# Kernel tuning notes

Measured on AMD Instinct MI355X. Metric: run time of the kernel, lower is better.

The kernel has to match this reference:

```python
import jax, jax.numpy as jnp
import numpy as np

N = 100000
F_IN = 128
H = 128
E = 1600000
EP = 200000


def _gcn_conv(x, W, b, src, dst, n):
    # GCNConv (PyG default): add self-loops done by caller; symmetric norm; linear + scatter-add.
    xw = x @ W                                        # [n, H]
    deg = jax.ops.segment_sum(jnp.ones(src.shape[0], x.dtype), dst, num_segments=n)
    dinv = jnp.where(deg > 0, jax.lax.rsqrt(deg), 0.0)
    norm = dinv[src] * dinv[dst]                      # [E']
    msg = xw[src] * norm[:, None]                     # [E', H] gather
    out = jax.ops.segment_sum(msg, dst, num_segments=n)  # scatter-add
    return out + b


def setup_inputs() -> dict:
    key = jax.random.key(0)
    k = jax.random.split(key, 9)
    x = jax.random.normal(k[0], (N, F_IN), dtype=jnp.float32)
    edge_index = jax.random.randint(k[1], (2, E), 0, N, dtype=jnp.int64)
    dict_node = jax.random.randint(k[2], (N,), 0, N, dtype=jnp.int64)
    pos_edge_index = jax.random.randint(k[3], (2, EP), 0, N, dtype=jnp.int64)
    neg_edge_index = jax.random.randint(k[4], (2, EP), 0, N, dtype=jnp.int64)
    s1 = 1.0 / np.sqrt(F_IN)
    s2 = 1.0 / np.sqrt(H)
    W1 = jax.random.uniform(k[5], (F_IN, H), jnp.float32, -s1, s1)
    b1 = jnp.zeros((H,), jnp.float32)
    W2 = jax.random.uniform(k[6], (H, H), jnp.float32, -s2, s2)
    b2 = jnp.zeros((H,), jnp.float32)
    return {"x": x, "W1": W1, "b1": b1, "W2": W2, "b2": b2,
            "edge_index": edge_index, "dict_node": dict_node,
            "pos_edge_index": pos_edge_index, "neg_edge_index": neg_edge_index}


def reference(x, W1, b1, W2, b2, edge_index, dict_node, pos_edge_index, neg_edge_index):
    n = x.shape[0]
    # add self-loops once (both convs use the same edge_index)
    loop = jnp.arange(n, dtype=edge_index.dtype)
    src = jnp.concatenate([edge_index[0], loop])
    dst = jnp.concatenate([edge_index[1], loop])
    # encode (dropout p=0.01 is identity in eval mode)
    h = jax.nn.relu(_gcn_conv(x, W1, b1, src, dst, n))
    h = jax.nn.relu(_gcn_conv(h, W2, b2, src, dst, n))
    # global_mean_pool over dict_node segments (size = num_nodes)
    sums = jax.ops.segment_sum(h, dict_node, num_segments=n)
    cnt = jax.ops.segment_sum(jnp.ones((n,), h.dtype), dict_node, num_segments=n)
    z = sums / jnp.maximum(cnt, 1.0)[:, None]
    # decode: per-edge dot products over concatenated pos/neg edges
    ei = jnp.concatenate([pos_edge_index, neg_edge_index], axis=-1)
    logits = jnp.sum(z[ei[0]] * z[ei[1]], axis=-1)
    return logits
```

## Files before the change

kernel.cpp:

```cpp
#include <hip/hip_runtime.h>
#include <hip/hip_fp16.h>

#define HH 128
#define PCHUNK 16384


__global__ __launch_bounds__(256) void part_count_k(const int* __restrict__ key, int e,
                                                    int nbkt, int nblk,
                                                    int* __restrict__ gcnt,
                                                    int* __restrict__ blkoff) {
  __shared__ int h[512];
  for (int i = threadIdx.x; i < nbkt; i += 256) h[i] = 0;
  __syncthreads();
  int start = blockIdx.x * PCHUNK;
  int cnt = e - start; if (cnt > PCHUNK) cnt = PCHUNK;
  for (int i = threadIdx.x; i < cnt; i += 256)
    atomicAdd(&h[key[start + i] >> 8], 1);
  __syncthreads();
  for (int i = threadIdx.x; i < nbkt; i += 256) {
    int c = h[i];
    if (c) blkoff[(size_t)i * nblk + blockIdx.x] = atomicAdd(&gcnt[i], c);
  }
}

__global__ __launch_bounds__(512) void scan_bkt_k(const int* __restrict__ gcnt,
                                                  int* __restrict__ bktbase, int nbkt, int e) {
  __shared__ int sc[512];
  int tid = threadIdx.x;
  int v = (tid < nbkt) ? gcnt[tid] : 0;
  sc[tid] = v;
  __syncthreads();
  for (int off = 1; off < 512; off <<= 1) {
    int t = (tid >= off) ? sc[tid - off] : 0;
    __syncthreads();
    sc[tid] += t;
    __syncthreads();
  }
  if (tid < nbkt) bktbase[tid] = sc[tid] - v;
  if (tid == 0) bktbase[nbkt] = e;
}

__global__ __launch_bounds__(256) void part_scatter_k(const int* __restrict__ src,
                                                      const int* __restrict__ key, int e,
                                                      int nbkt, int nblk,
                                                      const int* __restrict__ bktbase,
                                                      const int* __restrict__ blkoff,
                                                      int* __restrict__ part) {
  __shared__ int cur[512];
  for (int i = threadIdx.x; i < nbkt; i += 256)
    cur[i] = bktbase[i] + blkoff[(size_t)i * nblk + blockIdx.x];
  __syncthreads();
  int start = blockIdx.x * PCHUNK;
  int cnt = e - start; if (cnt > PCHUNK) cnt = PCHUNK;
  for (int i = threadIdx.x; i < cnt; i += 256) {
    int d = key[start + i], s = src[start + i];
    int pos = atomicAdd(&cur[d >> 8], 1);
    part[pos] = (s << 8) | (d & 255);
  }
}

__global__ __launch_bounds__(256) void part_scatter_idx_k(const int* __restrict__ key, int e,
                                                          int nbkt, int nblk,
                                                          const int* __restrict__ bktbase,
                                                          const int* __restrict__ blkoff,
                                                          int* __restrict__ part) {
  __shared__ int cur[512];
  for (int i = threadIdx.x; i < nbkt; i += 256)
    cur[i] = bktbase[i] + blkoff[(size_t)i * nblk + blockIdx.x];
  __syncthreads();
  int start = blockIdx.x * PCHUNK;
  int cnt = e - start; if (cnt > PCHUNK) cnt = PCHUNK;
  for (int i = threadIdx.x; i < cnt; i += 256) {
    int d = key[start + i];
    int pos = atomicAdd(&cur[d >> 8], 1);
    part[pos] = ((start + i) << 8) | (d & 255);
  }
}

__global__ __launch_bounds__(256) void bucket_csr_k(const int* __restrict__ part,
                                                    const int* __restrict__ bktbase,
                                                    int* __restrict__ rowptr,
                                                    float* __restrict__ dinv,
                                                    int* __restrict__ esrc,
                                                    int n, int e, int nbkt) {
  __shared__ int hist[256];
  __shared__ int sc[256];
  __shared__ int cur[256];
  int tid = threadIdx.x;
  int b = blockIdx.x;
  int dstbase = b << 8;
  int nloc = n - dstbase; if (nloc > 256) nloc = 256;
  int beg = bktbase[b], bend = bktbase[b + 1];

  hist[tid] = 0;
  __syncthreads();
  for (int j = beg + tid; j < bend; j += 256)
    atomicAdd(&hist[part[j] & 255], 1);
  __syncthreads();
  int v = hist[tid];
  sc[tid] = v;
  __syncthreads();
  for (int off = 1; off < 256; off <<= 1) {
    int t = (tid >= off) ? sc[tid - off] : 0;
    __syncthreads();
    sc[tid] += t;
    __syncthreads();
  }
  int excl = sc[tid] - v;
  if (tid < nloc) {
    rowptr[dstbase + tid] = beg + excl;
    cur[tid] = beg + excl;
    if (dinv) dinv[dstbase + tid] = rsqrtf((float)v + 1.0f);
  }
  __syncthreads();
  for (int j = beg + tid; j < bend; j += 256) {
    int p = part[j];
    int pos = atomicAdd(&cur[p & 255], 1);
    esrc[pos] = p >> 8;
  }
  if (b == nbkt - 1 && tid == 0) rowptr[n] = e;
}

template <bool OUT16>
__global__ __launch_bounds__(256) void gemm128_v4(const float* __restrict__ A,
                                                  const float* __restrict__ W,
                                                  const float* __restrict__ dscale,
                                                  void* __restrict__ out, int n) {
  __shared__ float As[64][65];
  const int tid = threadIdx.x;
  const int rbase = blockIdx.x * 64;
  const int vrows = (n - rbase) < 64 ? (n - rbase) : 64;

  const int r = tid & 63;
  const int q = __builtin_amdgcn_readfirstlane(tid >> 6);
  const float* Wq = W + q * 32;

  float4 acc[8];
  #pragma unroll
  for (int c = 0; c < 8; ++c) acc[c] = make_float4(0.f, 0.f, 0.f, 0.f);

  #pragma unroll
  for (int ph = 0; ph < 2; ++ph) {
    if (ph) __syncthreads();
    #pragma unroll
    for (int j = 0; j < 4; ++j) {
      int f = tid + 256 * j;
      int rr = f >> 4, c4 = f & 15;
      float4 v = (rr < vrows)
          ? ((const float4*)(A + (size_t)(rbase + rr) * HH + ph * 64))[c4]
          : make_float4(0.f, 0.f, 0.f, 0.f);
      As[rr][c4 * 4 + 0] = v.x;
      As[rr][c4 * 4 + 1] = v.y;
      As[rr][c4 * 4 + 2] = v.z;
      As[rr][c4 * 4 + 3] = v.w;
    }
    __syncthreads();

    #pragma unroll 4
    for (int kk = 0; kk < 64; ++kk) {
      float a = As[r][kk];
      const float4* Wr = (const float4*)(Wq + (size_t)(ph * 64 + kk) * HH);
      #pragma unroll
      for (int c = 0; c < 8; ++c) {
        float4 w = Wr[c];
        acc[c].x += a * w.x; acc[c].y += a * w.y;
        acc[c].z += a * w.z; acc[c].w += a * w.w;
      }
    }
  }

  int row = rbase + r;
  if (row < n) {
    float s = dscale ? dscale[row] : 1.0f;
    if (OUT16) {
      uint2* o = (uint2*)((__half*)out + (size_t)row * HH) + q * 8;
      #pragma unroll
      for (int c = 0; c < 8; ++c) {
        __half2 h0 = __float22half2_rn(make_float2(acc[c].x * s, acc[c].y * s));
        __half2 h1 = __float22half2_rn(make_float2(acc[c].z * s, acc[c].w * s));
        uint2 u;
        u.x = *reinterpret_cast<unsigned*>(&h0);
        u.y = *reinterpret_cast<unsigned*>(&h1);
        o[c] = u;
      }
    } else {
      float4* o = (float4*)((float*)out + (size_t)row * HH + q * 32);
      #pragma unroll
      for (int c = 0; c < 8; ++c) {
        acc[c].x *= s; acc[c].y *= s; acc[c].z *= s; acc[c].w *= s;
        o[c] = acc[c];
      }
    }
  }
}

template <bool HOUT16>
__global__ __launch_bounds__(256) void gather16_k(const __half* __restrict__ xw16,
                                                  const int* __restrict__ rowptr,
                                                  const int* __restrict__ esrc,
                                                  const float* __restrict__ dinv,
                                                  const float* __restrict__ bias,
                                                  void* __restrict__ h, int n) {
  int wid = (int)((blockIdx.x * (size_t)blockDim.x + threadIdx.x) >> 6);
  int lane = threadIdx.x & 63;
  if (wid >= n) return;
  int beg = rowptr[wid], end = rowptr[wid + 1];
  int half = lane >> 5, l32 = lane & 31;
  const uint2* base = (const uint2*)xw16 + l32;
  float4 acc = make_float4(0.f, 0.f, 0.f, 0.f);

  for (int j0 = beg; j0 < end; j0 += 64) {
    int myj = j0 + lane;
    int sv = (myj < end) ? esrc[myj] : 0;
    int cnt = end - j0; if (cnt > 64) cnt = 64;
    int k = 0;
    for (; k + 8 <= cnt; k += 8) {
      #pragma unroll
      for (int p = 0; p < 4; ++p) {
        int sa = __builtin_amdgcn_readlane(sv, k + 2 * p);
        int sb = __builtin_amdgcn_readlane(sv, k + 2 * p + 1);
        unsigned off = (unsigned)(half ? sb : sa) << 5;
        uint2 u = base[off];
        float2 f0 = __half22float2(*reinterpret_cast<__half2*>(&u.x));
        float2 f1 = __half22float2(*reinterpret_cast<__half2*>(&u.y));
        acc.x += f0.x; acc.y += f0.y; acc.z += f1.x; acc.w += f1.y;
      }
    }
    for (; k + 2 <= cnt; k += 2) {
      int sa = __builtin_amdgcn_readlane(sv, k);
      int sb = __builtin_amdgcn_readlane(sv, k + 1);
      unsigned off = (unsigned)(half ? sb : sa) << 5;
      uint2 u = base[off];
      float2 f0 = __half22float2(*reinterpret_cast<__half2*>(&u.x));
      float2 f1 = __half22float2(*reinterpret_cast<__half2*>(&u.y));
      acc.x += f0.x; acc.y += f0.y; acc.z += f1.x; acc.w += f1.y;
    }
    if (k < cnt) {
      int sa = __builtin_amdgcn_readlane(sv, k);
      if (half == 0) {
        uint2 u = base[(unsigned)sa << 5];
        float2 f0 = __half22float2(*reinterpret_cast<__half2*>(&u.x));
        float2 f1 = __half22float2(*reinterpret_cast<__half2*>(&u.y));
        acc.x += f0.x; acc.y += f0.y; acc.z += f1.x; acc.w += f1.y;
      }
    }
  }
  acc.x += __shfl_xor(acc.x, 32);
  acc.y += __shfl_xor(acc.y, 32);
  acc.z += __shfl_xor(acc.z, 32);
  acc.w += __shfl_xor(acc.w, 32);
  if (half == 0) {
    uint2 u = base[(unsigned)wid << 5];
    float2 s0 = __half22float2(*reinterpret_cast<__half2*>(&u.x));
    float2 s1 = __half22float2(*reinterpret_cast<__half2*>(&u.y));
    float di = dinv[wid];
    float4 bb = ((const float4*)bias)[l32];
    float4 o;
    o.x = fmaxf(bb.x + di * (acc.x + s0.x), 0.f);
    o.y = fmaxf(bb.y + di * (acc.y + s0.y), 0.f);
    o.z = fmaxf(bb.z + di * (acc.z + s1.x), 0.f);
    o.w = fmaxf(bb.w + di * (acc.w + s1.y), 0.f);
    if (HOUT16) {
      __half2 p0 = __float22half2_rn(make_float2(o.x, o.y));
      __half2 p1 = __float22half2_rn(make_float2(o.z, o.w));
      uint2 w;
      w.x = *reinterpret_cast<unsigned*>(&p0);
      w.y = *reinterpret_cast<unsigned*>(&p1);
      ((uint2*)h)[((size_t)wid << 5) + l32] = w;
    } else {
      ((float4*)h)[((size_t)wid << 5) + l32] = o;
    }
  }
}

__global__ __launch_bounds__(256) void pool16_k(const __half* __restrict__ h2,
                                                const int* __restrict__ rowptr,
                                                const int* __restrict__ nodelist,
                                                __half* __restrict__ z, int n) {
  int gid = blockIdx.x * blockDim.x + threadIdx.x;
  int g = gid >> 5, l32 = gid & 31;
  if (g >= n) return;
  int beg = rowptr[g], end = rowptr[g + 1];
  const uint2* h4 = (const uint2*)h2;
  float4 a = make_float4(0.f, 0.f, 0.f, 0.f);
  for (int j = beg; j < end; ++j) {
    int m = nodelist[j];
    uint2 u = h4[((size_t)m << 5) + l32];
    float2 f0 = __half22float2(*reinterpret_cast<__half2*>(&u.x));
    float2 f1 = __half22float2(*reinterpret_cast<__half2*>(&u.y));
    a.x += f0.x; a.y += f0.y; a.z += f1.x; a.w += f1.y;
  }
  float inv = 1.0f / fmaxf((float)(end - beg), 1.0f);
  __half2 p0 = __float22half2_rn(make_float2(a.x * inv, a.y * inv));
  __half2 p1 = __float22half2_rn(make_float2(a.z * inv, a.w * inv));
  uint2 w;
  w.x = *reinterpret_cast<unsigned*>(&p0);
  w.y = *reinterpret_cast<unsigned*>(&p1);
  ((uint2*)z)[((size_t)g << 5) + l32] = w;
}

__global__ __launch_bounds__(256) void decode16_k(const __half* __restrict__ z,
                                                  const int* __restrict__ pos,
                                                  const int* __restrict__ neg,
                                                  float* __restrict__ out, int ep) {
  int gid = blockIdx.x * blockDim.x + threadIdx.x;
  int edge = gid >> 5, l32 = gid & 31;
  if (edge >= 2 * ep) return;
  int a, b;
  if (edge < ep) { a = pos[edge];      b = pos[ep + edge]; }
  else           { int t = edge - ep; a = neg[t]; b = neg[ep + t]; }
  const uint2* z4 = (const uint2*)z;
  uint2 ua = z4[((size_t)a << 5) + l32];
  uint2 ub = z4[((size_t)b << 5) + l32];
  float2 fa0 = __half22float2(*reinterpret_cast<__half2*>(&ua.x));
  float2 fa1 = __half22float2(*reinterpret_cast<__half2*>(&ua.y));
  float2 fb0 = __half22float2(*reinterpret_cast<__half2*>(&ub.x));
  float2 fb1 = __half22float2(*reinterpret_cast<__half2*>(&ub.y));
  float dot = fa0.x * fb0.x + fa0.y * fb0.y + fa1.x * fb1.x + fa1.y * fb1.y;
  #pragma unroll
  for (int off = 16; off > 0; off >>= 1) dot += __shfl_xor(dot, off);
  if (l32 == 0) out[edge] = dot;
}

__global__ void fill_deg_k(float* __restrict__ deg, int n) {
  int i = blockIdx.x * blockDim.x + threadIdx.x;
  if (i < n) deg[i] = 1.0f;
}
__global__ void accum_deg_k(const int* __restrict__ dst, float* __restrict__ deg, int e) {
  int i = blockIdx.x * blockDim.x + threadIdx.x;
  if (i < e) atomicAdd(&deg[dst[i]], 1.0f);
}
__global__ void dinv_k(float* __restrict__ deg, int n) {
  int i = blockIdx.x * blockDim.x + threadIdx.x;
  if (i < n) deg[i] = rsqrtf(deg[i]);
}
__global__ void init_h_k(const float* __restrict__ xw, const float* __restrict__ bias,
                         const float* __restrict__ dinv, float* __restrict__ h, int n) {
  int gid = blockIdx.x * blockDim.x + threadIdx.x;
  int node = gid >> 5, c4 = gid & 31;
  if (node >= n) return;
  float di = dinv[node];
  float nm = di * di;
  float4 v = ((const float4*)(xw + (size_t)node * HH))[c4];
  float4 b = ((const float4*)bias)[c4];
  ((float4*)(h + (size_t)node * HH))[c4] =
      make_float4(b.x + nm * v.x, b.y + nm * v.y, b.z + nm * v.z, b.w + nm * v.w);
}
__global__ void scatter_k(const float* __restrict__ xw, float* __restrict__ h,
                          const float* __restrict__ dinv, const int* __restrict__ src,
                          const int* __restrict__ dst, int e) {
  int gid = blockIdx.x * blockDim.x + threadIdx.x;
  int edge = gid >> 5, lane = gid & 31;
  if (edge >= e) return;
  int s = src[edge], d = dst[edge];
  float norm = dinv[s] * dinv[d];
  float4 v = ((const float4*)(xw + (size_t)s * HH))[lane];
  float* o = h + (size_t)d * HH + lane * 4;
  atomicAdd(o + 0, norm * v.x);
  atomicAdd(o + 1, norm * v.y);
  atomicAdd(o + 2, norm * v.z);
  atomicAdd(o + 3, norm * v.w);
}
__global__ void relu_k(float4* __restrict__ h, int n4) {
  int i = blockIdx.x * blockDim.x + threadIdx.x;
  if (i < n4) {
    float4 v = h[i];
    v.x = fmaxf(v.x, 0.f); v.y = fmaxf(v.y, 0.f);
    v.z = fmaxf(v.z, 0.f); v.w = fmaxf(v.w, 0.f);
    h[i] = v;
  }
}
__global__ void pool_accum_k(const float* __restrict__ h, const int* __restrict__ dict,
                             float* __restrict__ z, float* __restrict__ cnt, int n) {
  int gid = blockIdx.x * blockDim.x + threadIdx.x;
  int node = gid >> 5, lane = gid & 31;
  if (node >= n) return;
  int d = dict[node];
  float4 v = ((const float4*)(h + (size_t)node * HH))[lane];
  float* o = z + (size_t)d * HH + lane * 4;
  atomicAdd(o + 0, v.x); atomicAdd(o + 1, v.y);
  atomicAdd(o + 2, v.z); atomicAdd(o + 3, v.w);
  if (lane == 0) atomicAdd(&cnt[d], 1.0f);
}
__global__ void pool_div_k(float* __restrict__ z, const float* __restrict__ cnt, int n) {
  int gid = blockIdx.x * blockDim.x + threadIdx.x;
  int node = gid >> 5, lane = gid & 31;
  if (node >= n) return;
  float inv = 1.0f / fmaxf(cnt[node], 1.0f);
  float4* p = (float4*)(z + (size_t)node * HH) + lane;
  float4 v = *p;
  v.x *= inv; v.y *= inv; v.z *= inv; v.w *= inv;
  *p = v;
}
__global__ void decode_k(const float* __restrict__ z, const int* __restrict__ pos,
                         const int* __restrict__ neg, float* __restrict__ out, int ep) {
  int gid = blockIdx.x * blockDim.x + threadIdx.x;
  int edge = gid >> 5, lane = gid & 31;
  if (edge >= 2 * ep) return;
  int a, b;
  if (edge < ep) { a = pos[edge];      b = pos[ep + edge]; }
  else           { a = neg[edge - ep]; b = neg[edge]; }
  const float4* za = (const float4*)(z + (size_t)a * HH);
  const float4* zb = (const float4*)(z + (size_t)b * HH);
  float4 va = za[lane], vb = zb[lane];
  float dot = va.x * vb.x + va.y * vb.y + va.z * vb.z + va.w * vb.w;
  #pragma unroll
  for (int off = 16; off > 0; off >>= 1) dot += __shfl_xor(dot, off);
  if (lane == 0) out[edge] = dot;
}

extern "C" void kernel_launch(void* const* d_in, const int* in_sizes, int n_in,
                              void* d_out, int out_size, void* d_ws, size_t ws_size,
                              hipStream_t stream) {
  const float* x  = (const float*)d_in[0];
  const float* W1 = (const float*)d_in[1];
  const float* b1 = (const float*)d_in[2];
  const float* W2 = (const float*)d_in[3];
  const float* b2 = (const float*)d_in[4];
  const int* ei   = (const int*)d_in[5];
  const int* dict = (const int*)d_in[6];
  const int* pe   = (const int*)d_in[7];
  const int* ne   = (const int*)d_in[8];

  const int n  = in_sizes[0] / HH;
  const int e  = in_sizes[5] / 2;
  const int ep = in_sizes[7] / 2;
  const int* src = ei;
  const int* dst = ei + e;

  const size_t nf = (size_t)n * HH;
  const int nbkt  = (n + 255) >> 8;
  const int nblkE = (e + PCHUNK - 1) / PCHUNK;
  const int nblkN = (n + PCHUNK - 1) / PCHUNK;

  float*  p0     = (float*)d_ws;
  float*  bufF   = p0;
  __half* xw16   = (__half*)(p0 + nf);
  float*  dinv   = p0 + nf + nf / 2;
  int*    rowptr = (int*)(dinv + n);
  int*    tmp    = rowptr + (n + 1);
  int*    esrc   = tmp + n;
  int*    bsum   = esrc + e;
  int*    gcnt   = bsum + 256;
  int*    bktbase = gcnt + nbkt;
  size_t need = (nf + nf / 2 + n) * sizeof(float) +
                (size_t)(3 * n + 1 + e + 256 + 2 * nbkt + 1) * sizeof(int);

  int* partE   = (int*)bufF;
  int* blkoffE = (int*)xw16;
  int* partN   = (int*)(bufF + nf / 2);
  int* blkoffN = partN + n;

  const int nb    = (n + 255) / 256;
  const int nb32  = (int)(((size_t)n * 32 + 255) / 256);
  const int nb64  = (int)(((size_t)n * 64 + 255) / 256);
  const int gemb  = (n + 63) / 64;
  const int deb   = (int)(((size_t)2 * ep * 32 + 255) / 256);

  bool fast = (ws_size >= need) && (nbkt <= 512) && (n < (1 << 23)) &&
              ((size_t)e <= nf) && ((size_t)nbkt * nblkE * 2 <= nf) &&
              ((size_t)(n + nbkt * nblkN) * 2 <= nf);

  if (fast) {
    hipMemsetAsync(gcnt, 0, (size_t)nbkt * sizeof(int), stream);
    part_count_k<<<nblkE, 256, 0, stream>>>(dst, e, nbkt, nblkE, gcnt, blkoffE);
    scan_bkt_k<<<1, 512, 0, stream>>>(gcnt, bktbase, nbkt, e);
    part_scatter_k<<<nblkE, 256, 0, stream>>>(src, dst, e, nbkt, nblkE, bktbase, blkoffE, partE);
    bucket_csr_k<<<nbkt, 256, 0, stream>>>(partE, bktbase, rowptr, dinv, esrc, n, e, nbkt);

    gemm128_v4<true><<<gemb, 256, 0, stream>>>(x, W1, dinv, xw16, n);
    gather16_k<false><<<nb64, 256, 0, stream>>>(xw16, rowptr, esrc, dinv, b1, bufF, n);
    gemm128_v4<true><<<gemb, 256, 0, stream>>>(bufF, W2, dinv, xw16, n);
    __half* h2_16 = (__half*)bufF;
    gather16_k<true><<<nb64, 256, 0, stream>>>(xw16, rowptr, esrc, dinv, b2, h2_16, n);

    hipMemsetAsync(gcnt, 0, (size_t)nbkt * sizeof(int), stream);
    part_count_k<<<nblkN, 256, 0, stream>>>(dict, n, nbkt, nblkN, gcnt, blkoffN);
    scan_bkt_k<<<1, 512, 0, stream>>>(gcnt, bktbase, nbkt, n);
    part_scatter_idx_k<<<nblkN, 256, 0, stream>>>(dict, n, nbkt, nblkN, bktbase, blkoffN, partN);
    bucket_csr_k<<<nbkt, 256, 0, stream>>>(partN, bktbase, rowptr, nullptr, esrc, n, n, nbkt);

    __half* z16 = xw16;
    pool16_k<<<nb32, 256, 0, stream>>>(h2_16, rowptr, esrc, z16, n);
    decode16_k<<<deb, 256, 0, stream>>>(z16, pe, ne, (float*)d_out, ep);
  } else {
    float* bufA  = (float*)d_ws;
    float* bufB  = bufA + nf;
    float* dinv2 = bufB + nf;
    float* cnt   = dinv2 + n;
    fill_deg_k<<<nb, 256, 0, stream>>>(dinv2, n);
    accum_deg_k<<<(e + 255) / 256, 256, 0, stream>>>(dst, dinv2, e);
    dinv_k<<<nb, 256, 0, stream>>>(dinv2, n);

    gemm128_v4<false><<<gemb, 256, 0, stream>>>(x, W1, nullptr, bufA, n);
    init_h_k<<<nb32, 256, 0, stream>>>(bufA, b1, dinv2, bufB, n);
    scatter_k<<<(int)(((size_t)e * 32 + 255) / 256), 256, 0, stream>>>(bufA, bufB, dinv2, src, dst, e);
    relu_k<<<nb32, 256, 0, stream>>>((float4*)bufB, n * 32);

    gemm128_v4<false><<<gemb, 256, 0, stream>>>(bufB, W2, nullptr, bufA, n);
    init_h_k<<<nb32, 256, 0, stream>>>(bufA, b2, dinv2, bufB, n);
    scatter_k<<<(int)(((size_t)e * 32 + 255) / 256), 256, 0, stream>>>(bufA, bufB, dinv2, src, dst, e);
    relu_k<<<nb32, 256, 0, stream>>>((float4*)bufB, n * 32);

    hipMemsetAsync(bufA, 0, nf * sizeof(float), stream);
    hipMemsetAsync(cnt, 0, (size_t)n * sizeof(float), stream);
    pool_accum_k<<<nb32, 256, 0, stream>>>(bufB, dict, bufA, cnt, n);
    pool_div_k<<<nb32, 256, 0, stream>>>(bufA, cnt, n);
    decode_k<<<(int)(((size_t)2 * ep * 32 + 255) / 256), 256, 0, stream>>>(
        bufA, pe, ne, (float*)d_out, ep);
  }
}
```

Baseline: 380.9 us.

## Store layer-1 activations in fp16, widen pool/decode loads, shrink node-partition chunk

The first GCN layer's output is now written as fp16 and the second GEMM reads fp16 input, converting it to float in shared memory. This halves that intermediate's write and read traffic at the cost of extra rounding. Pool and decode kernels now use 16 lanes with 128-bit loads per row instead of 32 lanes with 64-bit loads. The node-partition chunk size drops from 16384 to 2048 so the dict_node partitioning runs on more blocks.

```diff
diff --git a/kernel.cpp b/kernel.cpp
--- a/kernel.cpp
+++ b/kernel.cpp
@@ -1,19 +1,19 @@
 #include <hip/hip_runtime.h>
 #include <hip/hip_fp16.h>
+#include <type_traits>
 
 #define HH 128
-#define PCHUNK 16384
 
 
 __global__ __launch_bounds__(256) void part_count_k(const int* __restrict__ key, int e,
-                                                    int nbkt, int nblk,
+                                                    int chunk, int nbkt, int nblk,
                                                     int* __restrict__ gcnt,
                                                     int* __restrict__ blkoff) {
   __shared__ int h[512];
   for (int i = threadIdx.x; i < nbkt; i += 256) h[i] = 0;
   __syncthreads();
-  int start = blockIdx.x * PCHUNK;
-  int cnt = e - start; if (cnt > PCHUNK) cnt = PCHUNK;
+  int start = blockIdx.x * chunk;
+  int cnt = e - start; if (cnt > chunk) cnt = chunk;
   for (int i = threadIdx.x; i < cnt; i += 256)
     atomicAdd(&h[key[start + i] >> 8], 1);
   __syncthreads();
@@ -42,7 +42,7 @@
 
 __global__ __launch_bounds__(256) void part_scatter_k(const int* __restrict__ src,
                                                       const int* __restrict__ key, int e,
-                                                      int nbkt, int nblk,
+                                                      int chunk, int nbkt, int nblk,
                                                       const int* __restrict__ bktbase,
                                                       const int* __restrict__ blkoff,
                                                       int* __restrict__ part) {
@@ -50,8 +50,8 @@
   for (int i = threadIdx.x; i < nbkt; i += 256)
     cur[i] = bktbase[i] + blkoff[(size_t)i * nblk + blockIdx.x];
   __syncthreads();
-  int start = blockIdx.x * PCHUNK;
-  int cnt = e - start; if (cnt > PCHUNK) cnt = PCHUNK;
+  int start = blockIdx.x * chunk;
+  int cnt = e - start; if (cnt > chunk) cnt = chunk;
   for (int i = threadIdx.x; i < cnt; i += 256) {
     int d = key[start + i], s = src[start + i];
     int pos = atomicAdd(&cur[d >> 8], 1);
@@ -60,7 +60,7 @@
 }
 
 __global__ __launch_bounds__(256) void part_scatter_idx_k(const int* __restrict__ key, int e,
-                                                          int nbkt, int nblk,
+                                                          int chunk, int nbkt, int nblk,
                                                           const int* __restrict__ bktbase,
                                                           const int* __restrict__ blkoff,
                                                           int* __restrict__ part) {
@@ -68,8 +68,8 @@
   for (int i = threadIdx.x; i < nbkt; i += 256)
     cur[i] = bktbase[i] + blkoff[(size_t)i * nblk + blockIdx.x];
   __syncthreads();
-  int start = blockIdx.x * PCHUNK;
-  int cnt = e - start; if (cnt > PCHUNK) cnt = PCHUNK;
+  int start = blockIdx.x * chunk;
+  int cnt = e - start; if (cnt > chunk) cnt = chunk;
   for (int i = threadIdx.x; i < cnt; i += 256) {
     int d = key[start + i];
     int pos = atomicAdd(&cur[d >> 8], 1);
@@ -121,8 +121,8 @@
   if (b == nbkt - 1 && tid == 0) rowptr[n] = e;
 }
 
-template <bool OUT16>
-__global__ __launch_bounds__(256) void gemm128_v4(const float* __restrict__ A,
+template <typename TIN, bool OUT16>
+__global__ __launch_bounds__(256) void gemm128_v5(const TIN* __restrict__ A,
                                                   const float* __restrict__ W,
                                                   const float* __restrict__ dscale,
                                                   void* __restrict__ out, int n) {
@@ -142,17 +142,35 @@
   #pragma unroll
   for (int ph = 0; ph < 2; ++ph) {
     if (ph) __syncthreads();
-    #pragma unroll
-    for (int j = 0; j < 4; ++j) {
-      int f = tid + 256 * j;
-      int rr = f >> 4, c4 = f & 15;
-      float4 v = (rr < vrows)
-          ? ((const float4*)(A + (size_t)(rbase + rr) * HH + ph * 64))[c4]
-          : make_float4(0.f, 0.f, 0.f, 0.f);
-      As[rr][c4 * 4 + 0] = v.x;
-      As[rr][c4 * 4 + 1] = v.y;
-      As[rr][c4 * 4 + 2] = v.z;
-      As[rr][c4 * 4 + 3] = v.w;
+    if (std::is_same<TIN, __half>::value) {
+      #pragma unroll
+      for (int j = 0; j < 2; ++j) {
+        int f = tid + 256 * j;
+        int rr = f >> 3, c8 = f & 7;
+        uint4 u = make_uint4(0u, 0u, 0u, 0u);
+        if (rr < vrows)
+          u = ((const uint4*)((const __half*)A + (size_t)(rbase + rr) * HH + ph * 64))[c8];
+        __half2* hp = (__half2*)&u;
+        #pragma unroll
+        for (int t = 0; t < 4; ++t) {
+          float2 f2 = __half22float2(hp[t]);
+          As[rr][c8 * 8 + 2 * t + 0] = f2.x;
+          As[rr][c8 * 8 + 2 * t + 1] = f2.y;
+        }
+      }
+    } else {
+      #pragma unroll
+      for (int j = 0; j < 4; ++j) {
+        int f = tid + 256 * j;
+        int rr = f >> 4, c4 = f & 15;
+        float4 v = (rr < vrows)
+            ? ((const float4*)((const float*)A + (size_t)(rbase + rr) * HH + ph * 64))[c4]
+            : make_float4(0.f, 0.f, 0.f, 0.f);
+        As[rr][c4 * 4 + 0] = v.x;
+        As[rr][c4 * 4 + 1] = v.y;
+        As[rr][c4 * 4 + 2] = v.z;
+        As[rr][c4 * 4 + 3] = v.w;
+      }
     }
     __syncthreads();
 
@@ -278,25 +296,31 @@
                                                 const int* __restrict__ nodelist,
                                                 __half* __restrict__ z, int n) {
   int gid = blockIdx.x * blockDim.x + threadIdx.x;
-  int g = gid >> 5, l32 = gid & 31;
+  int g = gid >> 4, l16 = gid & 15;
   if (g >= n) return;
   int beg = rowptr[g], end = rowptr[g + 1];
-  const uint2* h4 = (const uint2*)h2;
-  float4 a = make_float4(0.f, 0.f, 0.f, 0.f);
+  const uint4* h4 = (const uint4*)h2;
+  float a[8];
+  #pragma unroll
+  for (int t = 0; t < 8; ++t) a[t] = 0.f;
   for (int j = beg; j < end; ++j) {
     int m = nodelist[j];
-    uint2 u = h4[((size_t)m << 5) + l32];
-    float2 f0 = __half22float2(*reinterpret_cast<__half2*>(&u.x));
-    float2 f1 = __half22float2(*reinterpret_cast<__half2*>(&u.y));
-    a.x += f0.x; a.y += f0.y; a.z += f1.x; a.w += f1.y;
+    uint4 u = h4[((size_t)m << 4) + l16];
+    __half2* hp = (__half2*)&u;
+    #pragma unroll
+    for (int t = 0; t < 4; ++t) {
+      float2 f2 = __half22float2(hp[t]);
+      a[2 * t + 0] += f2.x;
+      a[2 * t + 1] += f2.y;
+    }
   }
   float inv = 1.0f / fmaxf((float)(end - beg), 1.0f);
-  __half2 p0 = __float22half2_rn(make_float2(a.x * inv, a.y * inv));
-  __half2 p1 = __float22half2_rn(make_float2(a.z * inv, a.w * inv));
-  uint2 w;
-  w.x = *reinterpret_cast<unsigned*>(&p0);
-  w.y = *reinterpret_cast<unsigned*>(&p1);
-  ((uint2*)z)[((size_t)g << 5) + l32] = w;
+  uint4 w;
+  __half2* wp = (__half2*)&w;
+  #pragma unroll
+  for (int t = 0; t < 4; ++t)
+    wp[t] = __float22half2_rn(make_float2(a[2 * t] * inv, a[2 * t + 1] * inv));
+  ((uint4*)z)[((size_t)g << 4) + l16] = w;
 }
 
 __global__ __launch_bounds__(256) void decode16_k(const __half* __restrict__ z,
@@ -304,22 +328,26 @@
                                                   const int* __restrict__ neg,
                                                   float* __restrict__ out, int ep) {
   int gid = blockIdx.x * blockDim.x + threadIdx.x;
-  int edge = gid >> 5, l32 = gid & 31;
+  int edge = gid >> 4, l16 = gid & 15;
   if (edge >= 2 * ep) return;
   int a, b;
   if (edge < ep) { a = pos[edge];      b = pos[ep + edge]; }
   else           { int t = edge - ep; a = neg[t]; b = neg[ep + t]; }
-  const uint2* z4 = (const uint2*)z;
-  uint2 ua = z4[((size_t)a << 5) + l32];
-  uint2 ub = z4[((size_t)b << 5) + l32];
-  float2 fa0 = __half22float2(*reinterpret_cast<__half2*>(&ua.x));
-  float2 fa1 = __half22float2(*reinterpret_cast<__half2*>(&ua.y));
-  float2 fb0 = __half22float2(*reinterpret_cast<__half2*>(&ub.x));
-  float2 fb1 = __half22float2(*reinterpret_cast<__half2*>(&ub.y));
-  float dot = fa0.x * fb0.x + fa0.y * fb0.y + fa1.x * fb1.x + fa1.y * fb1.y;
-  #pragma unroll
-  for (int off = 16; off > 0; off >>= 1) dot += __shfl_xor(dot, off);
-  if (l32 == 0) out[edge] = dot;
+  const uint4* z4 = (const uint4*)z;
+  uint4 ua = z4[((size_t)a << 4) + l16];
+  uint4 ub = z4[((size_t)b << 4) + l16];
+  __half2* ha = (__half2*)&ua;
+  __half2* hb = (__half2*)&ub;
+  float dot = 0.f;
+  #pragma unroll
+  for (int t = 0; t < 4; ++t) {
+    float2 fa = __half22float2(ha[t]);
+    float2 fb = __half22float2(hb[t]);
+    dot += fa.x * fb.x + fa.y * fb.y;
+  }
+  #pragma unroll
+  for (int off = 8; off > 0; off >>= 1) dot += __shfl_xor(dot, off);
+  if (l16 == 0) out[edge] = dot;
 }
 
 __global__ void fill_deg_k(float* __restrict__ deg, int n) {
@@ -430,8 +458,9 @@
 
   const size_t nf = (size_t)n * HH;
   const int nbkt  = (n + 255) >> 8;
-  const int nblkE = (e + PCHUNK - 1) / PCHUNK;
-  const int nblkN = (n + PCHUNK - 1) / PCHUNK;
+  const int CHE   = 16384, CHN = 2048;
+  const int nblkE = (e + CHE - 1) / CHE;
+  const int nblkN = (n + CHN - 1) / CHN;
 
   float*  p0     = (float*)d_ws;
   float*  bufF   = p0;
@@ -452,37 +481,39 @@
   int* blkoffN = partN + n;
 
   const int nb    = (n + 255) / 256;
+  const int nb16  = (int)(((size_t)n * 16 + 255) / 256);
   const int nb32  = (int)(((size_t)n * 32 + 255) / 256);
   const int nb64  = (int)(((size_t)n * 64 + 255) / 256);
   const int gemb  = (n + 63) / 64;
-  const int deb   = (int)(((size_t)2 * ep * 32 + 255) / 256);
+  const int deb16 = (int)(((size_t)2 * ep * 16 + 255) / 256);
 
   bool fast = (ws_size >= need) && (nbkt <= 512) && (n < (1 << 23)) &&
               ((size_t)e <= nf) && ((size_t)nbkt * nblkE * 2 <= nf) &&
-              ((size_t)(n + nbkt * nblkN) * 2 <= nf);
+              ((size_t)(n + (size_t)nbkt * nblkN) * 2 <= nf);
 
   if (fast) {
     hipMemsetAsync(gcnt, 0, (size_t)nbkt * sizeof(int), stream);
-    part_count_k<<<nblkE, 256, 0, stream>>>(dst, e, nbkt, nblkE, gcnt, blkoffE);
+    part_count_k<<<nblkE, 256, 0, stream>>>(dst, e, CHE, nbkt, nblkE, gcnt, blkoffE);
     scan_bkt_k<<<1, 512, 0, stream>>>(gcnt, bktbase, nbkt, e);
-    part_scatter_k<<<nblkE, 256, 0, stream>>>(src, dst, e, nbkt, nblkE, bktbase, blkoffE, partE);
+    part_scatter_k<<<nblkE, 256, 0, stream>>>(src, dst, e, CHE, nbkt, nblkE, bktbase, blkoffE, partE);
     bucket_csr_k<<<nbkt, 256, 0, stream>>>(partE, bktbase, rowptr, dinv, esrc, n, e, nbkt);
 
-    gemm128_v4<true><<<gemb, 256, 0, stream>>>(x, W1, dinv, xw16, n);
-    gather16_k<false><<<nb64, 256, 0, stream>>>(xw16, rowptr, esrc, dinv, b1, bufF, n);
-    gemm128_v4<true><<<gemb, 256, 0, stream>>>(bufF, W2, dinv, xw16, n);
+    gemm128_v5<float, true><<<gemb, 256, 0, stream>>>(x, W1, dinv, xw16, n);
+    __half* h1_16 = (__half*)bufF;
+    gather16_k<true><<<nb64, 256, 0, stream>>>(xw16, rowptr, esrc, dinv, b1, h1_16, n);
+    gemm128_v5<__half, true><<<gemb, 256, 0, stream>>>(h1_16, W2, dinv, xw16, n);
     __half* h2_16 = (__half*)bufF;
     gather16_k<true><<<nb64, 256, 0, stream>>>(xw16, rowptr, esrc, dinv, b2, h2_16, n);
 
     hipMemsetAsync(gcnt, 0, (size_t)nbkt * sizeof(int), stream);
-    part_count_k<<<nblkN, 256, 0, stream>>>(dict, n, nbkt, nblkN, gcnt, blkoffN);
+    part_count_k<<<nblkN, 256, 0, stream>>>(dict, n, CHN, nbkt, nblkN, gcnt, blkoffN);
     scan_bkt_k<<<1, 512, 0, stream>>>(gcnt, bktbase, nbkt, n);
-    part_scatter_idx_k<<<nblkN, 256, 0, stream>>>(dict, n, nbkt, nblkN, bktbase, blkoffN, partN);
+    part_scatter_idx_k<<<nblkN, 256, 0, stream>>>(dict, n, CHN, nbkt, nblkN, bktbase, blkoffN, partN);
     bucket_csr_k<<<nbkt, 256, 0, stream>>>(partN, bktbase, rowptr, nullptr, esrc, n, n, nbkt);
 
     __half* z16 = xw16;
-    pool16_k<<<nb32, 256, 0, stream>>>(h2_16, rowptr, esrc, z16, n);
-    decode16_k<<<deb, 256, 0, stream>>>(z16, pe, ne, (float*)d_out, ep);
+    pool16_k<<<nb16, 256, 0, stream>>>(h2_16, rowptr, esrc, z16, n);
+    decode16_k<<<deb16, 256, 0, stream>>>(z16, pe, ne, (float*)d_out, ep);
   } else {
     float* bufA  = (float*)d_ws;
     float* bufB  = bufA + nf;
@@ -492,12 +523,12 @@
     accum_deg_k<<<(e + 255) / 256, 256, 0, stream>>>(dst, dinv2, e);
     dinv_k<<<nb, 256, 0, stream>>>(dinv2, n);
 
-    gemm128_v4<false><<<gemb, 256, 0, stream>>>(x, W1, nullptr, bufA, n);
+    gemm128_v5<float, false><<<gemb, 256, 0, stream>>>(x, W1, nullptr, bufA, n);
     init_h_k<<<nb32, 256, 0, stream>>>(bufA, b1, dinv2, bufB, n);
     scatter_k<<<(int)(((size_t)e * 32 + 255) / 256), 256, 0, stream>>>(bufA, bufB, dinv2, src, dst, e);
     relu_k<<<nb32, 256, 0, stream>>>((float4*)bufB, n * 32);
 
-    gemm128_v4<false><<<gemb, 256, 0, stream>>>(bufB, W2, nullptr, bufA, n);
+    gemm128_v5<float, false><<<gemb, 256, 0, stream>>>(bufB, W2, nullptr, bufA, n);
     init_h_k<<<nb32, 256, 0, stream>>>(bufA, b2, dinv2, bufB, n);
     scatter_k<<<(int)(((size_t)e * 32 + 255) / 256), 256, 0, stream>>>(bufA, bufB, dinv2, src, dst, e);
     relu_k<<<nb32, 256, 0, stream>>>((float4*)bufB, n * 32);
```

New measurement: 333.3 us. 1.14x faster.
